# Performance work log

Hardware: AMD Instinct MI355X
Metric: run time of the kernel (lower is better)

## Reference

```python
import jax, jax.numpy as jnp
import numpy as np

USER_SIZE = 1_000_000
ITEM_SIZE = 1_000_000
EMBED = 64
BATCH = 4096
NUM_TOTAL = 100
STD = 0.01


def setup_inputs() -> dict:
    key = jax.random.key(0)
    ks = jax.random.split(key, 16)
    d = {}
    d["user"] = jax.random.randint(ks[0], (BATCH, 1), 0, USER_SIZE, dtype=jnp.int64 if jax.config.jax_enable_x64 else jnp.int32)
    d["item"] = jax.random.randint(ks[1], (BATCH, NUM_TOTAL), 0, ITEM_SIZE, dtype=jnp.int64 if jax.config.jax_enable_x64 else jnp.int32)
    d["num_total"] = NUM_TOTAL
    # Embedding tables stored as [vocab, embed] (transpose of nn.Linear weight [embed, vocab])
    d["Wu_gmf"] = jax.random.normal(ks[2], (USER_SIZE, EMBED), jnp.float32) * STD
    d["bu_gmf"] = jnp.zeros((EMBED,), jnp.float32)
    d["Wu_mlp"] = jax.random.normal(ks[3], (USER_SIZE, EMBED), jnp.float32) * STD
    d["bu_mlp"] = jnp.zeros((EMBED,), jnp.float32)
    d["Wi_gmf"] = jax.random.normal(ks[4], (ITEM_SIZE, EMBED), jnp.float32) * STD
    d["bi_gmf"] = jnp.zeros((EMBED,), jnp.float32)
    d["Wi_mlp"] = jax.random.normal(ks[5], (ITEM_SIZE, EMBED), jnp.float32) * STD
    d["bi_mlp"] = jnp.zeros((EMBED,), jnp.float32)
    # MLP tower, stored as [in, out]
    d["W1"] = jax.random.normal(ks[6], (2 * EMBED, 2 * EMBED), jnp.float32) * STD
    d["b1"] = jnp.zeros((2 * EMBED,), jnp.float32)
    d["W2"] = jax.random.normal(ks[7], (2 * EMBED, EMBED), jnp.float32) * STD
    d["b2"] = jnp.zeros((EMBED,), jnp.float32)
    d["W3"] = jax.random.normal(ks[8], (EMBED, EMBED // 2), jnp.float32) * STD
    d["b3"] = jnp.zeros((EMBED // 2,), jnp.float32)
    d["Wp"] = jax.random.normal(ks[9], (3 * EMBED // 2, 1), jnp.float32) * STD
    d["bp"] = jnp.zeros((1,), jnp.float32)
    return d


def reference(user, item, num_total, Wu_gmf, bu_gmf, Wu_mlp, bu_mlp, Wi_gmf, bi_gmf, Wi_mlp, bi_mlp, W1, b1, W2, b2, W3, b3, Wp, bp):
    # one-hot @ Linear == embedding gather (column select of weight) + bias
    eu_g = Wu_gmf[user[:, 0]] + bu_gmf              # [B, E]
    eu_m = Wu_mlp[user[:, 0]] + bu_mlp              # [B, E]
    ei_g = Wi_gmf[item] + bi_gmf                    # [B, N, E]
    ei_m = Wi_mlp[item] + bi_mlp                    # [B, N, E]

    gmf = eu_g[:, None, :] * ei_g                   # [B, N, E]

    eu_m_b = jnp.broadcast_to(eu_m[:, None, :], ei_m.shape)
    inter = jnp.concatenate([eu_m_b, ei_m], axis=2)  # [B, N, 2E]
    h1 = jax.nn.relu(inter @ W1 + b1)
    h2 = jax.nn.relu(h1 @ W2 + b2)
    h3 = jax.nn.relu(h2 @ W3 + b3)                  # [B, N, E/2]

    concat = jnp.concatenate([gmf, h3], axis=2)     # [B, N, 3E/2]
    pred = jax.nn.sigmoid(concat @ Wp + bp)         # [B, N, 1]
    return pred[..., 0]                             # [B, N]
```

## Files before the change

### kernel.cpp

```cpp
#include <hip/hip_runtime.h>


typedef __attribute__((ext_vector_type(8))) short bf16x8;
typedef __attribute__((ext_vector_type(4))) float f32x4;

__device__ __forceinline__ short f2bf(float x){
  unsigned u = __float_as_uint(x);
  u += 0x7fffu + ((u >> 16) & 1u);
  return (short)(u >> 16);
}
__device__ __forceinline__ float bf2f(short s){
  return __uint_as_float(((unsigned)(unsigned short)s) << 16);
}


__global__ __launch_bounds__(256) void ncf_prep_w(
    const float* __restrict__ W1, const float* __restrict__ W2,
    const float* __restrict__ W3, const float* __restrict__ b1,
    const float* __restrict__ bi_mlp, short* __restrict__ ws,
    float* __restrict__ c1)
{
  if (blockIdx.x == 104){
    int j = threadIdx.x;
    if (j < 128){
      float acc = b1[j];
      #pragma unroll 4
      for (int k = 0; k < 64; k++)
        acc += bi_mlp[k] * W1[(64 + k)*128 + j];
      c1[j] = acc;
    }
    return;
  }
  int i = blockIdx.x * 256 + threadIdx.x;
  if (i < 8192){
    int col = i >> 6, k = i & 63;
    ws[i] = f2bf(W1[k*128 + col]);
  } else if (i < 16384){
    int t = i - 8192; int col = t >> 6, k = t & 63;
    ws[i] = f2bf(W1[(64 + k)*128 + col]);
  } else if (i < 24576){
    int t = i - 16384; int col = t >> 7, k = t & 127;
    ws[i] = f2bf(W2[k*64 + col]);
  } else if (i < 26624){
    int t = i - 24576; int col = t >> 6, k = t & 63;
    ws[i] = f2bf(W3[k*32 + col]);
  }
}

__global__ __launch_bounds__(256) void ncf_prep_u(
    const int* __restrict__ user,
    const float* __restrict__ Wu_gmf, const float* __restrict__ bu_gmf,
    const float* __restrict__ Wu_mlp, const float* __restrict__ bu_mlp,
    const float* __restrict__ bi_gmf, const float* __restrict__ Wp,
    const short* __restrict__ W1uT, const float* __restrict__ c1,
    float* __restrict__ Xu, float* __restrict__ wup, float* __restrict__ cu)
{
  __shared__ __align__(16) short s_eu[64][72];
  const int tid = threadIdx.x;
  const int r = tid >> 2, q = tid & 3;
  const int b = blockIdx.x * 64 + r;
  long u = (long)user[b];

  {
    const float4* ump = (const float4*)(Wu_mlp + u*64) + q*4;
    const float4* bmp = (const float4*)(bu_mlp) + q*4;
    const float4* ugp = (const float4*)(Wu_gmf + u*64) + q*4;
    const float4* bgp = (const float4*)(bu_gmf) + q*4;
    const float4* wpp = (const float4*)(Wp) + q*4;
    const float4* bip = (const float4*)(bi_gmf) + q*4;
    float4* wdst = (float4*)(wup + (long)b*64) + q*4;
    bf16x8 ea[2];
    float cacc = 0.f;
    #pragma unroll
    for (int j = 0; j < 4; j++){
      float4 m = ump[j], mb = bmp[j];
      int h = j >> 1, s = (j & 1) * 4;
      ea[h][s+0] = f2bf(m.x + mb.x); ea[h][s+1] = f2bf(m.y + mb.y);
      ea[h][s+2] = f2bf(m.z + mb.z); ea[h][s+3] = f2bf(m.w + mb.w);
      float4 g = ugp[j], gb = bgp[j], wp = wpp[j], bi = bip[j];
      float4 wg; wg.x = (g.x+gb.x)*wp.x; wg.y = (g.y+gb.y)*wp.y;
                 wg.z = (g.z+gb.z)*wp.z; wg.w = (g.w+gb.w)*wp.w;
      wdst[j] = wg;
      cacc += wg.x*bi.x + wg.y*bi.y + wg.z*bi.z + wg.w*bi.w;
    }
    *(bf16x8*)&s_eu[r][q*16]     = ea[0];
    *(bf16x8*)&s_eu[r][q*16 + 8] = ea[1];
    cacc += __shfl_xor(cacc, 1);
    cacc += __shfl_xor(cacc, 2);
    if (q == 0) cu[b] = cacc;
  }
  __syncthreads();

  const int w = tid >> 6, l = tid & 63, lr = l & 15, lg = l >> 4;
  f32x4 acc[4][2];
  #pragma unroll
  for (int mt = 0; mt < 4; mt++)
    #pragma unroll
    for (int nt = 0; nt < 2; nt++)
      acc[mt][nt] = (f32x4){0.f, 0.f, 0.f, 0.f};
  #pragma unroll
  for (int ks = 0; ks < 2; ks++){
    bf16x8 af[4];
    #pragma unroll
    for (int mt = 0; mt < 4; mt++)
      af[mt] = *(const bf16x8*)&s_eu[mt*16 + lr][ks*32 + lg*8];
    #pragma unroll
    for (int nt = 0; nt < 2; nt++){
      bf16x8 bf_ = *(const bf16x8*)&W1uT[(w*32 + nt*16 + lr)*64 + ks*32 + lg*8];
      #pragma unroll
      for (int mt = 0; mt < 4; mt++)
        acc[mt][nt] = __builtin_amdgcn_mfma_f32_16x16x32_bf16(af[mt], bf_, acc[mt][nt], 0, 0, 0);
    }
  }
  #pragma unroll
  for (int nt = 0; nt < 2; nt++){
    int col = w*32 + nt*16 + lr;
    float cc = c1[col];
    #pragma unroll
    for (int mt = 0; mt < 4; mt++)
      #pragma unroll
      for (int rr = 0; rr < 4; rr++){
        int row = mt*16 + lg*4 + rr;
        Xu[(long)(blockIdx.x*64 + row)*128 + col] = acc[mt][nt][rr] + cc;
      }
  }
}

__global__ __launch_bounds__(256) void ncf_main(
    const int* __restrict__ item,
    const float* __restrict__ Wi_mlp, const float* __restrict__ Wi_gmf,
    const short* __restrict__ W1iT, const short* __restrict__ W2T,
    const short* __restrict__ W3T,
    const float* __restrict__ b2, const float* __restrict__ b3,
    const float* __restrict__ Wp, const float* __restrict__ bp,
    const float* __restrict__ Xu, const float* __restrict__ wup,
    const float* __restrict__ cu,
    float* __restrict__ out, int N, int total, int ntiles, int Bsz)
{
  __shared__ __align__(16) short s_item[64][72];
  __shared__ __align__(16) short s_h1[64][136];
  __shared__ __align__(16) short s_h3[64][34];
  __shared__ __align__(16) float s_xu[2][128];
  __shared__           float s_pg[64];

  const int tid = threadIdx.x;
  const int r  = tid >> 2, q = tid & 3;
  const int w  = tid >> 6, l = tid & 63;
  const int lr = l & 15,  lg = l >> 4;
  const int G  = gridDim.x;

  bf16x8 w1f[2][2], w2f[4], w3f[2];
  #pragma unroll
  for (int nt = 0; nt < 2; nt++)
    #pragma unroll
    for (int ks = 0; ks < 2; ks++)
      w1f[nt][ks] = *(const bf16x8*)&W1iT[(w*32 + nt*16 + lr)*64 + ks*32 + lg*8];
  #pragma unroll
  for (int ks = 0; ks < 4; ks++)
    w2f[ks] = *(const bf16x8*)&W2T[(w*16 + lr)*128 + ks*32 + lg*8];
  #pragma unroll
  for (int ks = 0; ks < 2; ks++)
    w3f[ks] = *(const bf16x8*)&W3T[((w&1)*16 + lr)*64 + ks*32 + lg*8];

  for (int t = blockIdx.x; t < ntiles; t += G){
    const int p0  = t * 64;
    const int b0  = p0 / N;
    const int thr = (b0 + 1) * N;

    {
      int p = p0 + r;
      int bl = (p >= thr) ? 1 : 0;
      int b  = b0 + bl;
      long ib = (long)item[p] * 64;
      const float4* imp = (const float4*)(Wi_mlp + ib) + q*4;
      const float4* igp = (const float4*)(Wi_gmf + ib) + q*4;
      const float4* wq  = (const float4*)(wup + (long)b*64) + q*4;
      bf16x8 ia[2];
      float pg = 0.f;
      #pragma unroll
      for (int j = 0; j < 4; j++){
        float4 v = imp[j];
        float4 g = igp[j];
        float4 wv = wq[j];
        pg += g.x*wv.x + g.y*wv.y + g.z*wv.z + g.w*wv.w;
        int h = j >> 1, s = (j & 1) * 4;
        ia[h][s+0] = f2bf(v.x); ia[h][s+1] = f2bf(v.y);
        ia[h][s+2] = f2bf(v.z); ia[h][s+3] = f2bf(v.w);
      }
      *(bf16x8*)&s_item[r][q*16]     = ia[0];
      *(bf16x8*)&s_item[r][q*16 + 8] = ia[1];
      pg += __shfl_xor(pg, 1);
      pg += __shfl_xor(pg, 2);
      if (q == 0) s_pg[r] = pg + cu[b];
      int i2 = tid >> 7, col = tid & 127;
      int bb = b0 + i2; if (bb >= Bsz) bb = Bsz - 1;
      s_xu[i2][col] = Xu[(long)bb*128 + col];
    }
    __syncthreads();

    {
      f32x4 acc[4][2];
      #pragma unroll
      for (int mt = 0; mt < 4; mt++)
        #pragma unroll
        for (int nt = 0; nt < 2; nt++)
          acc[mt][nt] = (f32x4){0.f, 0.f, 0.f, 0.f};
      #pragma unroll
      for (int ks = 0; ks < 2; ks++){
        bf16x8 af[4];
        #pragma unroll
        for (int mt = 0; mt < 4; mt++)
          af[mt] = *(const bf16x8*)&s_item[mt*16 + lr][ks*32 + lg*8];
        #pragma unroll
        for (int nt = 0; nt < 2; nt++)
          #pragma unroll
          for (int mt = 0; mt < 4; mt++)
            acc[mt][nt] = __builtin_amdgcn_mfma_f32_16x16x32_bf16(af[mt], w1f[nt][ks], acc[mt][nt], 0, 0, 0);
      }
      #pragma unroll
      for (int nt = 0; nt < 2; nt++){
        int col = w*32 + nt*16 + lr;
        #pragma unroll
        for (int mt = 0; mt < 4; mt++)
          #pragma unroll
          for (int rr = 0; rr < 4; rr++){
            int row = mt*16 + lg*4 + rr;
            int bl = (p0 + row >= thr) ? 1 : 0;
            float v = acc[mt][nt][rr] + s_xu[bl][col];
            s_h1[row][col] = f2bf(v > 0.f ? v : 0.f);
          }
      }
    }
    __syncthreads();

    {
      f32x4 acc2[4];
      #pragma unroll
      for (int mt = 0; mt < 4; mt++) acc2[mt] = (f32x4){0.f, 0.f, 0.f, 0.f};
      #pragma unroll
      for (int ks = 0; ks < 4; ks++)
        #pragma unroll
        for (int mt = 0; mt < 4; mt++){
          bf16x8 a = *(const bf16x8*)&s_h1[mt*16 + lr][ks*32 + lg*8];
          acc2[mt] = __builtin_amdgcn_mfma_f32_16x16x32_bf16(a, w2f[ks], acc2[mt], 0, 0, 0);
        }
      int col = w*16 + lr;
      float bb = b2[col];
      #pragma unroll
      for (int mt = 0; mt < 4; mt++)
        #pragma unroll
        for (int rr = 0; rr < 4; rr++){
          int row = mt*16 + lg*4 + rr;
          float v = acc2[mt][rr] + bb;
          s_item[row][col] = f2bf(v > 0.f ? v : 0.f);
        }
    }
    __syncthreads();

    if (w < 2){
      f32x4 acc3[4];
      #pragma unroll
      for (int mt = 0; mt < 4; mt++) acc3[mt] = (f32x4){0.f, 0.f, 0.f, 0.f};
      #pragma unroll
      for (int ks = 0; ks < 2; ks++)
        #pragma unroll
        for (int mt = 0; mt < 4; mt++){
          bf16x8 a = *(const bf16x8*)&s_item[mt*16 + lr][ks*32 + lg*8];
          acc3[mt] = __builtin_amdgcn_mfma_f32_16x16x32_bf16(a, w3f[ks], acc3[mt], 0, 0, 0);
        }
      int col = w*16 + lr;
      float bb = b3[col];
      #pragma unroll
      for (int mt = 0; mt < 4; mt++)
        #pragma unroll
        for (int rr = 0; rr < 4; rr++){
          int row = mt*16 + lg*4 + rr;
          float v = acc3[mt][rr] + bb;
          s_h3[row][col] = f2bf(v > 0.f ? v : 0.f);
        }
    }
    __syncthreads();

    {
      float sum = 0.f;
      #pragma unroll
      for (int i = 0; i < 8; i++){
        int c = q*8 + i;
        sum += bf2f(s_h3[r][c]) * Wp[64 + c];
      }
      sum += __shfl_xor(sum, 1);
      sum += __shfl_xor(sum, 2);
      int p = p0 + r;
      if (q == 0 && p < total){
        float z = s_pg[r] + sum + bp[0];
        out[p] = 1.f / (1.f + __expf(-z));
      }
    }
    __syncthreads();
  }
}

extern "C" void kernel_launch(void* const* d_in, const int* in_sizes, int n_in,
                              void* d_out, int out_size, void* d_ws, size_t ws_size,
                              hipStream_t stream)
{
  const int*   user   = (const int*)  d_in[0];
  const int*   item   = (const int*)  d_in[1];
  const float* Wu_gmf = (const float*)d_in[3];
  const float* bu_gmf = (const float*)d_in[4];
  const float* Wu_mlp = (const float*)d_in[5];
  const float* bu_mlp = (const float*)d_in[6];
  const float* Wi_gmf = (const float*)d_in[7];
  const float* bi_gmf = (const float*)d_in[8];
  const float* Wi_mlp = (const float*)d_in[9];
  const float* bi_mlp = (const float*)d_in[10];
  const float* W1     = (const float*)d_in[11];
  const float* b1     = (const float*)d_in[12];
  const float* W2     = (const float*)d_in[13];
  const float* b2     = (const float*)d_in[14];
  const float* W3     = (const float*)d_in[15];
  const float* b3     = (const float*)d_in[16];
  const float* Wp     = (const float*)d_in[17];
  const float* bp     = (const float*)d_in[18];

  int B     = in_sizes[0];
  int total = in_sizes[1];
  int N     = total / B;

  char* wsb = (char*)d_ws;
  short* W1uT = (short*)wsb;
  short* W1iT = (short*)(wsb + 16384);
  short* W2T  = (short*)(wsb + 32768);
  short* W3T  = (short*)(wsb + 49152);
  float* c1   = (float*)(wsb + 53248);
  float* Xu   = (float*)(wsb + 57344);
  float* wup  = Xu  + (size_t)B * 128;
  float* cuv  = wup + (size_t)B * 64;

  ncf_prep_w<<<105, 256, 0, stream>>>(W1, W2, W3, b1, bi_mlp, (short*)d_ws, c1);
  ncf_prep_u<<<B/64, 256, 0, stream>>>(user, Wu_gmf, bu_gmf, Wu_mlp, bu_mlp,
                                       bi_gmf, Wp, W1uT, c1, Xu, wup, cuv);

  int ntiles = (total + 63) / 64;
  ncf_main<<<1024, 256, 0, stream>>>(item, Wi_mlp, Wi_gmf,
      W1iT, W2T, W3T, b2, b3, Wp, bp, Xu, wup, cuv,
      (float*)d_out, N, total, ntiles, B);
}
```

Measured before the change: 85.60 us.

## Switch MLP tower to FP8 MFMA with one tile per block

The item-side MLP matmuls now use FP8 weights and activations with fp8 MFMA instead of bf16, and operands are swapped so the weights act as the A operand. The persistent 1024-block loop is replaced by one block per 64-row tile. The W3 layer is fused with the final Wp dot product in registers, which removes the h3 shared buffer and one barrier. The aims are to halve the bytes for operands and LDS, raise matrix throughput and cut synchronisation, at the cost of FP8 precision error and reloading the weights from global memory in every block.

New measurement: 71.69 us. 16.2% less time.

```diff
diff --git a/kernel.cpp b/kernel.cpp
--- a/kernel.cpp
+++ b/kernel.cpp
@@ -9,16 +9,15 @@
   u += 0x7fffu + ((u >> 16) & 1u);
   return (short)(u >> 16);
 }
-__device__ __forceinline__ float bf2f(short s){
-  return __uint_as_float(((unsigned)(unsigned short)s) << 16);
+__device__ __forceinline__ unsigned char f2fp8(float x){
+  return (unsigned char)(__builtin_amdgcn_cvt_pk_fp8_f32(x, 0.f, 0, false) & 0xFF);
 }
 
 
 __global__ __launch_bounds__(256) void ncf_prep_w(
     const float* __restrict__ W1, const float* __restrict__ W2,
     const float* __restrict__ W3, const float* __restrict__ b1,
-    const float* __restrict__ bi_mlp, short* __restrict__ ws,
-    float* __restrict__ c1)
+    const float* __restrict__ bi_mlp, char* __restrict__ ws)
 {
   if (blockIdx.x == 104){
     int j = threadIdx.x;
@@ -27,23 +26,23 @@
       #pragma unroll 4
       for (int k = 0; k < 64; k++)
         acc += bi_mlp[k] * W1[(64 + k)*128 + j];
-      c1[j] = acc;
+      ((float*)(ws + 34816))[j] = acc;
     }
     return;
   }
   int i = blockIdx.x * 256 + threadIdx.x;
   if (i < 8192){
     int col = i >> 6, k = i & 63;
-    ws[i] = f2bf(W1[k*128 + col]);
+    ((short*)ws)[i] = f2bf(W1[k*128 + col]);
   } else if (i < 16384){
     int t = i - 8192; int col = t >> 6, k = t & 63;
-    ws[i] = f2bf(W1[(64 + k)*128 + col]);
+    ((unsigned char*)(ws + 16384))[t] = f2fp8(W1[(64 + k)*128 + col]);
   } else if (i < 24576){
     int t = i - 16384; int col = t >> 7, k = t & 127;
-    ws[i] = f2bf(W2[k*64 + col]);
-  } else if (i < 26624){
+    ((unsigned char*)(ws + 24576))[t] = f2fp8(W2[k*64 + col]);
+  } else {
     int t = i - 24576; int col = t >> 6, k = t & 63;
-    ws[i] = f2bf(W3[k*32 + col]);
+    ((unsigned char*)(ws + 32768))[t] = f2fp8(W3[k*32 + col]);
   }
 }
 
@@ -60,7 +59,6 @@
   const int r = tid >> 2, q = tid & 3;
   const int b = blockIdx.x * 64 + r;
   long u = (long)user[b];
-
   {
     const float4* ump = (const float4*)(Wu_mlp + u*64) + q*4;
     const float4* bmp = (const float4*)(bu_mlp) + q*4;
@@ -129,174 +127,161 @@
 __global__ __launch_bounds__(256) void ncf_main(
     const int* __restrict__ item,
     const float* __restrict__ Wi_mlp, const float* __restrict__ Wi_gmf,
-    const short* __restrict__ W1iT, const short* __restrict__ W2T,
-    const short* __restrict__ W3T,
+    const unsigned char* __restrict__ W1iT, const unsigned char* __restrict__ W2T,
+    const unsigned char* __restrict__ W3T,
     const float* __restrict__ b2, const float* __restrict__ b3,
     const float* __restrict__ Wp, const float* __restrict__ bp,
     const float* __restrict__ Xu, const float* __restrict__ wup,
     const float* __restrict__ cu,
-    float* __restrict__ out, int N, int total, int ntiles, int Bsz)
+    float* __restrict__ out, int N, int total, int Bsz)
 {
-  __shared__ __align__(16) short s_item[64][72];
-  __shared__ __align__(16) short s_h1[64][136];
-  __shared__ __align__(16) short s_h3[64][34];
+  __shared__ __align__(16) unsigned char s_item[64][80];
+  __shared__ __align__(16) unsigned char s_h1[64][136];
+  __shared__ __align__(16) unsigned char s_h2[64][80];
   __shared__ __align__(16) float s_xu[2][128];
-  __shared__           float s_pg[64];
+  __shared__            float s_pg[64];
 
   const int tid = threadIdx.x;
-  const int r  = tid >> 2, q = tid & 3;
-  const int w  = tid >> 6, l = tid & 63;
-  const int lr = l & 15,  lg = l >> 4;
-  const int G  = gridDim.x;
-
-  bf16x8 w1f[2][2], w2f[4], w3f[2];
-  #pragma unroll
-  for (int nt = 0; nt < 2; nt++)
-    #pragma unroll
-    for (int ks = 0; ks < 2; ks++)
-      w1f[nt][ks] = *(const bf16x8*)&W1iT[(w*32 + nt*16 + lr)*64 + ks*32 + lg*8];
-  #pragma unroll
-  for (int ks = 0; ks < 4; ks++)
-    w2f[ks] = *(const bf16x8*)&W2T[(w*16 + lr)*128 + ks*32 + lg*8];
-  #pragma unroll
-  for (int ks = 0; ks < 2; ks++)
-    w3f[ks] = *(const bf16x8*)&W3T[((w&1)*16 + lr)*64 + ks*32 + lg*8];
-
-  for (int t = blockIdx.x; t < ntiles; t += G){
-    const int p0  = t * 64;
-    const int b0  = p0 / N;
-    const int thr = (b0 + 1) * N;
-
-    {
-      int p = p0 + r;
-      int bl = (p >= thr) ? 1 : 0;
-      int b  = b0 + bl;
-      long ib = (long)item[p] * 64;
-      const float4* imp = (const float4*)(Wi_mlp + ib) + q*4;
-      const float4* igp = (const float4*)(Wi_gmf + ib) + q*4;
-      const float4* wq  = (const float4*)(wup + (long)b*64) + q*4;
-      bf16x8 ia[2];
-      float pg = 0.f;
-      #pragma unroll
-      for (int j = 0; j < 4; j++){
-        float4 v = imp[j];
-        float4 g = igp[j];
-        float4 wv = wq[j];
-        pg += g.x*wv.x + g.y*wv.y + g.z*wv.z + g.w*wv.w;
-        int h = j >> 1, s = (j & 1) * 4;
-        ia[h][s+0] = f2bf(v.x); ia[h][s+1] = f2bf(v.y);
-        ia[h][s+2] = f2bf(v.z); ia[h][s+3] = f2bf(v.w);
-      }
-      *(bf16x8*)&s_item[r][q*16]     = ia[0];
-      *(bf16x8*)&s_item[r][q*16 + 8] = ia[1];
-      pg += __shfl_xor(pg, 1);
-      pg += __shfl_xor(pg, 2);
-      if (q == 0) s_pg[r] = pg + cu[b];
-      int i2 = tid >> 7, col = tid & 127;
-      int bb = b0 + i2; if (bb >= Bsz) bb = Bsz - 1;
-      s_xu[i2][col] = Xu[(long)bb*128 + col];
-    }
-    __syncthreads();
-
-    {
-      f32x4 acc[4][2];
-      #pragma unroll
-      for (int mt = 0; mt < 4; mt++)
+  const int p0  = blockIdx.x * 64;
+  const int b0  = p0 / N;
+  const int thr = (b0 + 1) * N;
+  const int r   = tid >> 2, q = tid & 3;
+  const int w   = tid >> 6, l = tid & 63;
+  const int lr  = l & 15,  lg = l >> 4;
+  const float bp0 = bp[0];
+
+  {
+    int p = p0 + r;
+    int b = b0 + ((p >= thr) ? 1 : 0);
+    long ib = (long)item[p] * 64;
+    const float4* mp = (const float4*)(Wi_mlp + ib) + q*4;
+    const float4* gp = (const float4*)(Wi_gmf + ib) + q*4;
+    const float4* wq = (const float4*)(wup + (long)b*64) + q*4;
+    float pg = 0.f;
+    int pk[4];
+    #pragma unroll
+    for (int j = 0; j < 4; j++){
+      float4 m = mp[j], g = gp[j], wv = wq[j];
+      pg += g.x*wv.x + g.y*wv.y + g.z*wv.z + g.w*wv.w;
+      int t_ = __builtin_amdgcn_cvt_pk_fp8_f32(m.x, m.y, 0, false);
+      t_     = __builtin_amdgcn_cvt_pk_fp8_f32(m.z, m.w, t_, true);
+      pk[j] = t_;
+    }
+    *(int4*)&s_item[r][q*16] = (int4){pk[0], pk[1], pk[2], pk[3]};
+    pg += __shfl_xor(pg, 1);
+    pg += __shfl_xor(pg, 2);
+    if (q == 0) s_pg[r] = pg + cu[b];
+    int i2 = tid >> 7, col = tid & 127;
+    int bb = b0 + i2; if (bb >= Bsz) bb = Bsz - 1;
+    s_xu[i2][col] = Xu[(long)bb*128 + col];
+  }
+  __syncthreads();
+
+  {
+    f32x4 acc[2][4];
+    #pragma unroll
+    for (int mt = 0; mt < 2; mt++)
+      #pragma unroll
+      for (int nt = 0; nt < 4; nt++)
+        acc[mt][nt] = (f32x4){0.f, 0.f, 0.f, 0.f};
+    #pragma unroll
+    for (int ks = 0; ks < 2; ks++){
+      long bfrag[4];
+      #pragma unroll
+      for (int nt = 0; nt < 4; nt++)
+        bfrag[nt] = *(const long*)&s_item[nt*16 + lr][ks*32 + lg*8];
+      #pragma unroll
+      for (int mt = 0; mt < 2; mt++){
+        long af = *(const long*)&W1iT[((w*2 + mt)*16 + lr)*64 + ks*32 + lg*8];
         #pragma unroll
-        for (int nt = 0; nt < 2; nt++)
-          acc[mt][nt] = (f32x4){0.f, 0.f, 0.f, 0.f};
-      #pragma unroll
-      for (int ks = 0; ks < 2; ks++){
-        bf16x8 af[4];
-        #pragma unroll
-        for (int mt = 0; mt < 4; mt++)
-          af[mt] = *(const bf16x8*)&s_item[mt*16 + lr][ks*32 + lg*8];
-        #pragma unroll
-        for (int nt = 0; nt < 2; nt++)
-          #pragma unroll
-          for (int mt = 0; mt < 4; mt++)
-            acc[mt][nt] = __builtin_amdgcn_mfma_f32_16x16x32_bf16(af[mt], w1f[nt][ks], acc[mt][nt], 0, 0, 0);
-      }
-      #pragma unroll
-      for (int nt = 0; nt < 2; nt++){
-        int col = w*32 + nt*16 + lr;
-        #pragma unroll
-        for (int mt = 0; mt < 4; mt++)
-          #pragma unroll
-          for (int rr = 0; rr < 4; rr++){
-            int row = mt*16 + lg*4 + rr;
-            int bl = (p0 + row >= thr) ? 1 : 0;
-            float v = acc[mt][nt][rr] + s_xu[bl][col];
-            s_h1[row][col] = f2bf(v > 0.f ? v : 0.f);
-          }
-      }
-    }
-    __syncthreads();
-
-    {
-      f32x4 acc2[4];
-      #pragma unroll
-      for (int mt = 0; mt < 4; mt++) acc2[mt] = (f32x4){0.f, 0.f, 0.f, 0.f};
-      #pragma unroll
-      for (int ks = 0; ks < 4; ks++)
-        #pragma unroll
-        for (int mt = 0; mt < 4; mt++){
-          bf16x8 a = *(const bf16x8*)&s_h1[mt*16 + lr][ks*32 + lg*8];
-          acc2[mt] = __builtin_amdgcn_mfma_f32_16x16x32_bf16(a, w2f[ks], acc2[mt], 0, 0, 0);
-        }
-      int col = w*16 + lr;
-      float bb = b2[col];
-      #pragma unroll
-      for (int mt = 0; mt < 4; mt++)
-        #pragma unroll
-        for (int rr = 0; rr < 4; rr++){
-          int row = mt*16 + lg*4 + rr;
-          float v = acc2[mt][rr] + bb;
-          s_item[row][col] = f2bf(v > 0.f ? v : 0.f);
-        }
-    }
-    __syncthreads();
-
-    if (w < 2){
-      f32x4 acc3[4];
-      #pragma unroll
-      for (int mt = 0; mt < 4; mt++) acc3[mt] = (f32x4){0.f, 0.f, 0.f, 0.f};
-      #pragma unroll
-      for (int ks = 0; ks < 2; ks++)
-        #pragma unroll
-        for (int mt = 0; mt < 4; mt++){
-          bf16x8 a = *(const bf16x8*)&s_item[mt*16 + lr][ks*32 + lg*8];
-          acc3[mt] = __builtin_amdgcn_mfma_f32_16x16x32_bf16(a, w3f[ks], acc3[mt], 0, 0, 0);
-        }
-      int col = w*16 + lr;
-      float bb = b3[col];
-      #pragma unroll
-      for (int mt = 0; mt < 4; mt++)
-        #pragma unroll
-        for (int rr = 0; rr < 4; rr++){
-          int row = mt*16 + lg*4 + rr;
-          float v = acc3[mt][rr] + bb;
-          s_h3[row][col] = f2bf(v > 0.f ? v : 0.f);
-        }
-    }
-    __syncthreads();
-
-    {
-      float sum = 0.f;
-      #pragma unroll
-      for (int i = 0; i < 8; i++){
-        int c = q*8 + i;
-        sum += bf2f(s_h3[r][c]) * Wp[64 + c];
-      }
-      sum += __shfl_xor(sum, 1);
-      sum += __shfl_xor(sum, 2);
-      int p = p0 + r;
-      if (q == 0 && p < total){
-        float z = s_pg[r] + sum + bp[0];
+        for (int nt = 0; nt < 4; nt++)
+          acc[mt][nt] = __builtin_amdgcn_mfma_f32_16x16x32_fp8_fp8(af, bfrag[nt], acc[mt][nt], 0, 0, 0);
+      }
+    }
+    #pragma unroll
+    for (int mt = 0; mt < 2; mt++){
+      int colb = (w*2 + mt)*16 + lg*4;
+      #pragma unroll
+      for (int nt = 0; nt < 4; nt++){
+        int pair = nt*16 + lr;
+        int bl = (p0 + pair >= thr) ? 1 : 0;
+        float4 xv = *(const float4*)&s_xu[bl][colb];
+        float v0 = acc[mt][nt][0] + xv.x; v0 = v0 > 0.f ? v0 : 0.f;
+        float v1 = acc[mt][nt][1] + xv.y; v1 = v1 > 0.f ? v1 : 0.f;
+        float v2 = acc[mt][nt][2] + xv.z; v2 = v2 > 0.f ? v2 : 0.f;
+        float v3 = acc[mt][nt][3] + xv.w; v3 = v3 > 0.f ? v3 : 0.f;
+        int t_ = __builtin_amdgcn_cvt_pk_fp8_f32(v0, v1, 0, false);
+        t_     = __builtin_amdgcn_cvt_pk_fp8_f32(v2, v3, t_, true);
+        *(int*)&s_h1[pair][colb] = t_;
+      }
+    }
+  }
+  __syncthreads();
+
+  {
+    f32x4 acc[4];
+    #pragma unroll
+    for (int nt = 0; nt < 4; nt++) acc[nt] = (f32x4){0.f, 0.f, 0.f, 0.f};
+    #pragma unroll
+    for (int ks = 0; ks < 4; ks++){
+      long af = *(const long*)&W2T[(w*16 + lr)*128 + ks*32 + lg*8];
+      #pragma unroll
+      for (int nt = 0; nt < 4; nt++){
+        long bf_ = *(const long*)&s_h1[nt*16 + lr][ks*32 + lg*8];
+        acc[nt] = __builtin_amdgcn_mfma_f32_16x16x32_fp8_fp8(af, bf_, acc[nt], 0, 0, 0);
+      }
+    }
+    int colb = w*16 + lg*4;
+    float4 b2v = *(const float4*)&b2[colb];
+    #pragma unroll
+    for (int nt = 0; nt < 4; nt++){
+      int pair = nt*16 + lr;
+      float v0 = acc[nt][0] + b2v.x; v0 = v0 > 0.f ? v0 : 0.f;
+      float v1 = acc[nt][1] + b2v.y; v1 = v1 > 0.f ? v1 : 0.f;
+      float v2 = acc[nt][2] + b2v.z; v2 = v2 > 0.f ? v2 : 0.f;
+      float v3 = acc[nt][3] + b2v.w; v3 = v3 > 0.f ? v3 : 0.f;
+      int t_ = __builtin_amdgcn_cvt_pk_fp8_f32(v0, v1, 0, false);
+      t_     = __builtin_amdgcn_cvt_pk_fp8_f32(v2, v3, t_, true);
+      *(int*)&s_h2[pair][colb] = t_;
+    }
+  }
+  __syncthreads();
+
+  {
+    f32x4 acc[2];
+    #pragma unroll
+    for (int mt = 0; mt < 2; mt++) acc[mt] = (f32x4){0.f, 0.f, 0.f, 0.f};
+    #pragma unroll
+    for (int ks = 0; ks < 2; ks++){
+      long bf_ = *(const long*)&s_h2[w*16 + lr][ks*32 + lg*8];
+      #pragma unroll
+      for (int mt = 0; mt < 2; mt++){
+        long af = *(const long*)&W3T[(mt*16 + lr)*64 + ks*32 + lg*8];
+        acc[mt] = __builtin_amdgcn_mfma_f32_16x16x32_fp8_fp8(af, bf_, acc[mt], 0, 0, 0);
+      }
+    }
+    float t = 0.f;
+    #pragma unroll
+    for (int mt = 0; mt < 2; mt++){
+      int colb = mt*16 + lg*4;
+      float4 b3v = *(const float4*)&b3[colb];
+      float4 wpv = *(const float4*)&Wp[64 + colb];
+      float v0 = acc[mt][0] + b3v.x; v0 = v0 > 0.f ? v0 : 0.f;
+      float v1 = acc[mt][1] + b3v.y; v1 = v1 > 0.f ? v1 : 0.f;
+      float v2 = acc[mt][2] + b3v.z; v2 = v2 > 0.f ? v2 : 0.f;
+      float v3 = acc[mt][3] + b3v.w; v3 = v3 > 0.f ? v3 : 0.f;
+      t += v0*wpv.x + v1*wpv.y + v2*wpv.z + v3*wpv.w;
+    }
+    t += __shfl_xor(t, 16);
+    t += __shfl_xor(t, 32);
+    if (l < 16){
+      int pair = w*16 + l;
+      int p = p0 + pair;
+      if (p < total){
+        float z = t + s_pg[pair] + bp0;
         out[p] = 1.f / (1.f + __expf(-z));
       }
     }
-    __syncthreads();
   }
 }
 
@@ -328,21 +313,21 @@
   int N     = total / B;
 
   char* wsb = (char*)d_ws;
-  short* W1uT = (short*)wsb;
-  short* W1iT = (short*)(wsb + 16384);
-  short* W2T  = (short*)(wsb + 32768);
-  short* W3T  = (short*)(wsb + 49152);
-  float* c1   = (float*)(wsb + 53248);
-  float* Xu   = (float*)(wsb + 57344);
-  float* wup  = Xu  + (size_t)B * 128;
-  float* cuv  = wup + (size_t)B * 64;
-
-  ncf_prep_w<<<105, 256, 0, stream>>>(W1, W2, W3, b1, bi_mlp, (short*)d_ws, c1);
+  short*         W1uT = (short*)wsb;
+  unsigned char* W1iT = (unsigned char*)(wsb + 16384);
+  unsigned char* W2T  = (unsigned char*)(wsb + 24576);
+  unsigned char* W3T  = (unsigned char*)(wsb + 32768);
+  float*         c1   = (float*)(wsb + 34816);
+  float*         Xu   = (float*)(wsb + 36864);
+  float*         wup  = Xu  + (size_t)B * 128;
+  float*         cuv  = wup + (size_t)B * 64;
+
+  ncf_prep_w<<<105, 256, 0, stream>>>(W1, W2, W3, b1, bi_mlp, wsb);
   ncf_prep_u<<<B/64, 256, 0, stream>>>(user, Wu_gmf, bu_gmf, Wu_mlp, bu_mlp,
                                        bi_gmf, Wp, W1uT, c1, Xu, wup, cuv);
 
-  int ntiles = (total + 63) / 64;
-  ncf_main<<<1024, 256, 0, stream>>>(item, Wi_mlp, Wi_gmf,
+  int nblk = (total + 63) / 64;
+  ncf_main<<<nblk, 256, 0, stream>>>(item, Wi_mlp, Wi_gmf,
       W1iT, W2T, W3T, b2, b3, Wp, bp, Xu, wup, cuv,
-      (float*)d_out, N, total, ntiles, B);
-}
+      (float*)d_out, N, total, B);
+}
```
